# Performance work log

Measured on AMD Instinct MI355X. Metric: run time of the kernel, lower is better.

The kernel has to match this reference:

```python
import jax, jax.numpy as jnp
import numpy as np

B, N, DIM = 2, 2048, 512
HEADS, DIM_HEAD = 8, 64
INNER = HEADS * DIM_HEAD  # 512
SCALE = DIM_HEAD ** -0.5


def setup_inputs() -> dict:
    key = jax.random.key(0)
    k1, k2, k3, k4, k5 = jax.random.split(key, 5)
    s = 0.02
    return {
        "x1": jax.random.normal(k1, (B, N, DIM), jnp.float32),
        "x2": jax.random.normal(k2, (B, N, DIM), jnp.float32),
        "W_qk": jax.random.normal(k3, (DIM, 2 * INNER), jnp.float32) * s,
        "W_v": jax.random.normal(k4, (DIM, INNER), jnp.float32) * s,
        "W_out": jax.random.normal(k5, (INNER, DIM), jnp.float32) * s,
        "b_out": jnp.zeros((DIM,), jnp.float32),
    }


def _split_heads(t):
    # [b, n, h*d] -> [b, h, n, d]
    b, n, _ = t.shape
    return t.reshape(b, n, HEADS, DIM_HEAD).transpose(0, 2, 1, 3)


def reference(x1, x2, W_qk, W_v, W_out, b_out):
    # to_qk(x1) -> chunk into k, v ; to_v(x2) -> q  (names in orig are swapped)
    kv = x1 @ W_qk                      # [b, n1, 2*inner]
    k, v = jnp.split(kv, 2, axis=-1)
    q = x2 @ W_v                        # [b, n2, inner]
    q, k, v = _split_heads(q), _split_heads(k), _split_heads(v)  # [b,h,n,d]
    dots = jnp.einsum("bhid,bhjd->bhij", q, k) * SCALE  # [b,h,n2,n1]
    attn = jax.nn.softmax(dots, axis=-1)
    out = jnp.einsum("bhij,bhjd->bhid", attn, v)         # [b,h,n2,d]
    out = out.transpose(0, 2, 1, 3).reshape(out.shape[0], out.shape[2], INNER)
    return out @ W_out + b_out          # [b, n2, dim]
```

## Files before the change

kernel.cpp:

```cpp
#include <hip/hip_runtime.h>

typedef short bf16x8 __attribute__((ext_vector_type(8)));
typedef short bf16x4 __attribute__((ext_vector_type(4)));
typedef float f32x4 __attribute__((ext_vector_type(4)));
typedef float f32x16 __attribute__((ext_vector_type(16)));
typedef unsigned short u16;
typedef unsigned int u32;
typedef u16 u16x8 __attribute__((ext_vector_type(8)));
typedef u16 u16x4 __attribute__((ext_vector_type(4)));

#define DEV __device__ __forceinline__

DEV u16 f2bf(float f) {
  unsigned u = __float_as_uint(f);
  u += 0x7fff + ((u >> 16) & 1);
  return (u16)(u >> 16);
}

DEV int pkbf(float lo, float hi) {
  return __builtin_amdgcn_perm(__float_as_uint(hi) + 0x8000u,
                               __float_as_uint(lo) + 0x8000u, 0x07060302u);
}

#define MFMA16(a, b, c) __builtin_amdgcn_mfma_f32_16x16x32_bf16(a, b, c, 0, 0, 0)
#define MFMA3216(a, b, c) __builtin_amdgcn_mfma_f32_32x32x16_bf16(a, b, c, 0, 0, 0)

#if __has_builtin(__builtin_amdgcn_mfma_f32_32x32x8bf16_1k)
#define HAVE_PV8 1
#define PVMFMA(a, b, c) __builtin_amdgcn_mfma_f32_32x32x8bf16_1k(a, b, c, 0, 0, 0)
#else
#define HAVE_PV8 0
#endif

#if __has_builtin(__builtin_amdgcn_exp2f)
#define QSCALE 0.18033688011112042f
#define EXPFN(x) __builtin_amdgcn_exp2f(x)
#else
#define QSCALE 0.125f
#define EXPFN(x) __expf(x)
#endif

#define GLD16(gp, lp)                                                     \
  __builtin_amdgcn_global_load_lds(                                       \
      (const __attribute__((address_space(1))) u32*)(gp),                 \
      (__attribute__((address_space(3))) u32*)(lp), 16, 0, 0)

#define WAIT_VM0 __builtin_amdgcn_s_waitcnt(0x0F70)
#define WAIT_LGKM0 __builtin_amdgcn_s_waitcnt(0xC07F)

__global__ __launch_bounds__(256) void wprep(
    const float* __restrict__ Wqk, const float* __restrict__ Wv,
    const float* __restrict__ Wout,
    u16* __restrict__ WqkT, u16* __restrict__ WvT, u16* __restrict__ WoutT) {
  __shared__ float tf[32][33];
  int bx = blockIdx.x, t = threadIdx.x;
  const float* src; u16* dst; int Ncols; int id;
  if (bx < 512)      { id = bx;       src = Wqk;  dst = WqkT;  Ncols = 1024; }
  else if (bx < 768) { id = bx - 512; src = Wv;   dst = WvT;   Ncols = 512; }
  else               { id = bx - 768; src = Wout; dst = WoutT; Ncols = 512; }
  int tilesPerRow = Ncols >> 5;
  int tr = id / tilesPerRow, tc = id % tilesPerRow;
  int r0 = tr * 32, c0 = tc * 32;
  {
    int r = t >> 3, c4 = (t & 7) * 4;
    float4 v = *(const float4*)(src + (long)(r0 + r) * Ncols + c0 + c4);
    tf[r][c4] = v.x; tf[r][c4 + 1] = v.y; tf[r][c4 + 2] = v.z; tf[r][c4 + 3] = v.w;
  }
  __syncthreads();
  {
    int c = t >> 3, r4 = (t & 7) * 4;
    u16x4 o;
    o[0] = f2bf(tf[r4][c]); o[1] = f2bf(tf[r4 + 1][c]);
    o[2] = f2bf(tf[r4 + 2][c]); o[3] = f2bf(tf[r4 + 3][c]);
    *(u16x4*)(dst + (long)(c0 + c) * 512 + r0 + r4) = o;
  }
}

__global__ __launch_bounds__(256) void qkv_gemm(
    const float* __restrict__ x1, const float* __restrict__ x2,
    const u16* __restrict__ WqkT, const u16* __restrict__ WvT,
    u16* __restrict__ out_q, u16* __restrict__ out_k, u16* __restrict__ out_vt) {
  __shared__ u16 sA[2][128 * 40];
  __shared__ u16 sB[2][64 * 40];
  int bx = blockIdx.x, t = threadIdx.x;
  bool isQ = bx < 256;
  int bx2 = isQ ? bx : bx - 256;
  const float* Ap = isQ ? x2 : x1;
  const u16* BT = isQ ? WvT : WqkT;
  int m0 = (bx2 & 31) * 128, n0 = (bx2 >> 5) * 64;
  int w = t >> 6, l = t & 63, lm = l & 15, lq = l >> 4;

  f32x4 zero = {0.f, 0.f, 0.f, 0.f};
  f32x4 acc[2][4];
#pragma unroll
  for (int i = 0; i < 2; ++i)
#pragma unroll
    for (int j = 0; j < 4; ++j) acc[i][j] = zero;

  int sm = t >> 2;
  int skc = (t & 3) * 8;
  const float* gAf = Ap + (long)(m0 + sm) * 512 + skc;
  const u16* gB = BT + (long)(n0 + sm) * 512 + skc;

  auto loadA = [&](int kt, int rows) {
    long off = (long)rows * 512 + kt * 32;
    float4 f0 = *(const float4*)(gAf + off);
    float4 f1 = *(const float4*)(gAf + off + 4);
    bf16x8 o;
    o[0] = (short)f2bf(f0.x); o[1] = (short)f2bf(f0.y);
    o[2] = (short)f2bf(f0.z); o[3] = (short)f2bf(f0.w);
    o[4] = (short)f2bf(f1.x); o[5] = (short)f2bf(f1.y);
    o[6] = (short)f2bf(f1.z); o[7] = (short)f2bf(f1.w);
    return o;
  };

  bf16x8 a0 = loadA(0, 0);
  bf16x8 a1 = loadA(0, 64);
  bf16x8 b0 = *(const bf16x8*)(gB);
  *(bf16x8*)(sA[0] + sm * 40 + skc) = a0;
  *(bf16x8*)(sA[0] + (sm + 64) * 40 + skc) = a1;
  *(bf16x8*)(sB[0] + sm * 40 + skc) = b0;
  __syncthreads();

  for (int kt = 0; kt < 16; ++kt) {
    int cur = kt & 1;
    if (kt < 15) {
      a0 = loadA(kt + 1, 0);
      a1 = loadA(kt + 1, 64);
      b0 = *(const bf16x8*)(gB + (kt + 1) * 32);
    }
    bf16x8 af[2], bfr[4];
    af[0] = *(const bf16x8*)(sA[cur] + (w * 32 + lm) * 40 + lq * 8);
    af[1] = *(const bf16x8*)(sA[cur] + (w * 32 + 16 + lm) * 40 + lq * 8);
#pragma unroll
    for (int s = 0; s < 4; ++s)
      bfr[s] = *(const bf16x8*)(sB[cur] + (s * 16 + lm) * 40 + lq * 8);
#pragma unroll
    for (int ms = 0; ms < 2; ++ms)
#pragma unroll
      for (int s = 0; s < 4; ++s)
        acc[ms][s] = MFMA16(af[ms], bfr[s], acc[ms][s]);
    if (kt < 15) {
      int nxt = 1 - cur;
      *(bf16x8*)(sA[nxt] + sm * 40 + skc) = a0;
      *(bf16x8*)(sA[nxt] + (sm + 64) * 40 + skc) = a1;
      *(bf16x8*)(sB[nxt] + sm * 40 + skc) = b0;
    }
    __syncthreads();
  }

#pragma unroll
  for (int ms = 0; ms < 2; ++ms) {
    int gmBase = m0 + w * 32 + ms * 16 + lq * 4;
#pragma unroll
    for (int s = 0; s < 4; ++s) {
      int gc = n0 + s * 16 + lm;
      int b = gmBase >> 11, n = gmBase & 2047;
      if (isQ) {
#pragma unroll
        for (int r = 0; r < 4; ++r)
          out_q[(((long)(b << 3) + (gc >> 6)) * 2048 + n + r) * 64 + (gc & 63)] =
              f2bf(acc[ms][s][r] * QSCALE);
      } else if (gc < 512) {
#pragma unroll
        for (int r = 0; r < 4; ++r)
          out_k[(((long)(b << 3) + (gc >> 6)) * 2048 + n + r) * 64 + (gc & 63)] =
              f2bf(acc[ms][s][r]);
      } else {
        int c = gc - 512, h = c >> 6, d = c & 63;
        u16x4 vv;
#pragma unroll
        for (int r = 0; r < 4; ++r) vv[r] = f2bf(acc[ms][s][r]);
        *(u16x4*)(out_vt + (((long)(b << 3) + h) * 64 + d) * 2048 + n) = vv;
      }
    }
  }
}

__global__ __launch_bounds__(256, 4) void attn(
    const u16* __restrict__ Q, const u16* __restrict__ K,
    const u16* __restrict__ Vt, u16* __restrict__ O) {
  int id = blockIdx.x;
  int bh = id & 15, qt = id >> 4;
  int b = bh >> 3, h = bh & 7;
  const u16* Kh = K + (long)bh * 2048 * 64;
  const u16* Vh = Vt + (long)bh * 64 * 2048;
  int t = threadIdx.x, w = t >> 6, lane = t & 63, ln = lane & 31, hi = lane >> 5;

  __shared__ u16 smem[4][2][2048];
  u16* ktile = smem[w][0];
  u16* vtile = smem[w][1];

  bf16x8 qf[4];
  {
    const u16* qp = Q + (long)bh * 2048 * 64 + (long)(qt * 32 + ln) * 64 + hi * 8;
#pragma unroll
    for (int dc = 0; dc < 4; ++dc) qf[dc] = *(const bf16x8*)(qp + dc * 16);
  }

  f32x16 accO[2];
#pragma unroll
  for (int dt = 0; dt < 2; ++dt)
#pragma unroll
    for (int i = 0; i < 16; ++i) accO[dt][i] = 0.f;
  float dacc = 0.f;

  int l8 = lane & 7, lr8 = lane >> 3;
  int l4 = lane & 3, lr16 = lane >> 2;
  const u16* gK0 = Kh + (long)(w * 512 + lr8) * 64 + (l8 ^ lr8) * 8;
  const u16* gV0 = Vh + (long)lr16 * 2048 + w * 512 + (l4 ^ (lr16 & 3)) * 8;

  auto stage = [&](int jt) {
    const u16* gk = gK0 + (long)jt * 2048;
    const u16* gv = gV0 + jt * 32;
#pragma unroll
    for (int i = 0; i < 4; ++i) {
      GLD16(gk + i * 512, ktile + i * 512);
      GLD16(gv + (long)i * 32768, vtile + i * 512);
    }
  };

  stage(0);
  WAIT_VM0;

  int s7 = ln & 7, s3 = ln & 3;
  for (int jt = 0; jt < 16; ++jt) {
    f32x16 st1, st2;
#pragma unroll
    for (int i = 0; i < 16; ++i) { st1[i] = 0.f; st2[i] = 0.f; }
    bf16x8 kf0 = *(const bf16x8*)(ktile + ln * 64 + ((0 * 2 + hi) ^ s7) * 8);
    bf16x8 kf1 = *(const bf16x8*)(ktile + ln * 64 + ((1 * 2 + hi) ^ s7) * 8);
    bf16x8 kf2 = *(const bf16x8*)(ktile + ln * 64 + ((2 * 2 + hi) ^ s7) * 8);
    bf16x8 kf3 = *(const bf16x8*)(ktile + ln * 64 + ((3 * 2 + hi) ^ s7) * 8);
    st1 = MFMA3216(kf0, qf[0], st1);
    st2 = MFMA3216(kf1, qf[1], st2);
    st1 = MFMA3216(kf2, qf[2], st1);
    st2 = MFMA3216(kf3, qf[3], st2);

    float p[16];
#pragma unroll
    for (int i = 0; i < 16; ++i) {
      float e = EXPFN(st1[i] + st2[i]);
      p[i] = e;
      dacc += e;
    }

#if HAVE_PV8
#pragma unroll
    for (int c = 0; c < 4; ++c) {
      union { int2 i2; bf16x4 v; } u;
      u.i2.x = pkbf(p[c * 4 + 0], p[c * 4 + 1]);
      u.i2.y = pkbf(p[c * 4 + 2], p[c * 4 + 3]);
#pragma unroll
      for (int dt = 0; dt < 2; ++dt) {
        bf16x4 vf = *(const bf16x4*)(vtile + (dt * 32 + ln) * 32 +
                                     ((c ^ s3) * 8) + hi * 4);
        accO[dt] = PVMFMA(vf, u.v, accO[dt]);
      }
    }
#else
#pragma unroll
    for (int c2 = 0; c2 < 2; ++c2) {
      int o0x = pkbf(p[c2 * 8 + 0], p[c2 * 8 + 1]);
      int o0y = pkbf(p[c2 * 8 + 2], p[c2 * 8 + 3]);
      int o1x = pkbf(p[c2 * 8 + 4], p[c2 * 8 + 5]);
      int o1y = pkbf(p[c2 * 8 + 6], p[c2 * 8 + 7]);
      int s0x = __shfl_xor(o0x, 32), s0y = __shfl_xor(o0y, 32);
      int s1x = __shfl_xor(o1x, 32), s1y = __shfl_xor(o1y, 32);
      union { int4 i4; bf16x8 v; } u;
      if (hi) { u.i4.x = s1x; u.i4.y = s1y; u.i4.z = o1x; u.i4.w = o1y; }
      else    { u.i4.x = o0x; u.i4.y = o0y; u.i4.z = s0x; u.i4.w = s0y; }
#pragma unroll
      for (int dt = 0; dt < 2; ++dt) {
        bf16x8 vf = *(const bf16x8*)(vtile + (dt * 32 + ln) * 32 +
                                     (((c2 * 2 + hi) ^ s3) * 8));
        accO[dt] = MFMA3216(vf, u.v, accO[dt]);
      }
    }
#endif

    if (jt < 15) {
      WAIT_LGKM0;
      stage(jt + 1);
      WAIT_VM0;
    }
  }

  __syncthreads();
  float* cb = (float*)&smem[0][0][0];
  if (w != 0) {
    float* sc = cb + (w - 1) * 2112;
#pragma unroll
    for (int dt = 0; dt < 2; ++dt)
#pragma unroll
      for (int i = 0; i < 16; ++i)
        sc[(dt * 16 + i) * 64 + hi * 32 + ln] = accO[dt][i];
    sc[2048 + hi * 32 + ln] = dacc;
  }
  __syncthreads();
  if (w == 0) {
#pragma unroll
    for (int j = 0; j < 3; ++j) {
      float* sc = cb + j * 2112;
#pragma unroll
      for (int dt = 0; dt < 2; ++dt)
#pragma unroll
        for (int i = 0; i < 16; ++i)
          accO[dt][i] += sc[(dt * 16 + i) * 64 + hi * 32 + ln];
      dacc += sc[2048 + hi * 32 + ln];
    }
    dacc += __shfl_xor(dacc, 32);
    float inv = 1.f / dacc;

    u16* Ob = O + ((long)b * 2048 + qt * 32 + ln) * 512 + h * 64;
#pragma unroll
    for (int dt = 0; dt < 2; ++dt)
#pragma unroll
      for (int gq = 0; gq < 4; ++gq) {
        u16x4 o;
#pragma unroll
        for (int rr = 0; rr < 4; ++rr) o[rr] = f2bf(accO[dt][gq * 4 + rr] * inv);
        *(u16x4*)(Ob + dt * 32 + gq * 8 + hi * 4) = o;
      }
  }
}

__global__ __launch_bounds__(128) void out_gemm(
    const u16* __restrict__ A, const u16* __restrict__ BT,
    float* __restrict__ out_f, const float* __restrict__ bias) {
  __shared__ u16 sA[2][64 * 40];
  __shared__ u16 sB[2][32 * 40];
  int t = threadIdx.x, bx = blockIdx.x;
  int m0 = (bx & 63) * 64, n0 = (bx >> 6) * 32;
  int w = t >> 6, l = t & 63, lm = l & 15, lq = l >> 4;

  f32x4 zero = {0.f, 0.f, 0.f, 0.f};
  f32x4 acc[2][2];
#pragma unroll
  for (int i = 0; i < 2; ++i)
#pragma unroll
    for (int j = 0; j < 2; ++j) acc[i][j] = zero;

  int ar = t >> 1, akc = (t & 1) * 16;
  int br = t >> 2, bkc = (t & 3) * 8;
  const u16* gA = A + (long)(m0 + ar) * 512 + akc;
  const u16* gB = BT + (long)(n0 + br) * 512 + bkc;

  bf16x8 a0 = *(const bf16x8*)(gA);
  bf16x8 a1 = *(const bf16x8*)(gA + 8);
  bf16x8 b0 = *(const bf16x8*)(gB);
  *(bf16x8*)(sA[0] + ar * 40 + akc) = a0;
  *(bf16x8*)(sA[0] + ar * 40 + akc + 8) = a1;
  *(bf16x8*)(sB[0] + br * 40 + bkc) = b0;
  __syncthreads();

  for (int kt = 0; kt < 16; ++kt) {
    int cur = kt & 1;
    if (kt < 15) {
      a0 = *(const bf16x8*)(gA + (kt + 1) * 32);
      a1 = *(const bf16x8*)(gA + (kt + 1) * 32 + 8);
      b0 = *(const bf16x8*)(gB + (kt + 1) * 32);
    }
    bf16x8 af[2], bfr[2];
    af[0] = *(const bf16x8*)(sA[cur] + (w * 32 + lm) * 40 + lq * 8);
    af[1] = *(const bf16x8*)(sA[cur] + (w * 32 + 16 + lm) * 40 + lq * 8);
    bfr[0] = *(const bf16x8*)(sB[cur] + (lm)*40 + lq * 8);
    bfr[1] = *(const bf16x8*)(sB[cur] + (16 + lm) * 40 + lq * 8);
#pragma unroll
    for (int ms = 0; ms < 2; ++ms)
#pragma unroll
      for (int s = 0; s < 2; ++s)
        acc[ms][s] = MFMA16(af[ms], bfr[s], acc[ms][s]);
    if (kt < 15) {
      int nxt = 1 - cur;
      *(bf16x8*)(sA[nxt] + ar * 40 + akc) = a0;
      *(bf16x8*)(sA[nxt] + ar * 40 + akc + 8) = a1;
      *(bf16x8*)(sB[nxt] + br * 40 + bkc) = b0;
    }
    __syncthreads();
  }

#pragma unroll
  for (int ms = 0; ms < 2; ++ms) {
    int gmBase = m0 + w * 32 + ms * 16 + lq * 4;
#pragma unroll
    for (int s = 0; s < 2; ++s) {
      int gc = n0 + s * 16 + lm;
      float bv = bias[gc];
#pragma unroll
      for (int r = 0; r < 4; ++r)
        out_f[(long)(gmBase + r) * 512 + gc] = acc[ms][s][r] + bv;
    }
  }
}

extern "C" void kernel_launch(void* const* d_in, const int* in_sizes, int n_in,
                              void* d_out, int out_size, void* d_ws, size_t ws_size,
                              hipStream_t stream) {
  const float* x1 = (const float*)d_in[0];
  const float* x2 = (const float*)d_in[1];
  const float* Wqk = (const float*)d_in[2];
  const float* Wv = (const float*)d_in[3];
  const float* Wout = (const float*)d_in[4];
  const float* bout = (const float*)d_in[5];
  float* out = (float*)d_out;

  u16* ws = (u16*)d_ws;
  const long SZ = 2097152;
  u16* Qw = ws;
  u16* Kw = ws + SZ;
  u16* Vtw = ws + 2 * SZ;
  u16* Ow = ws + 3 * SZ;
  u16* WqkT = ws + 4 * SZ;
  u16* WvT = WqkT + 524288;
  u16* WoutT = WvT + 262144;

  wprep<<<1024, 256, 0, stream>>>(Wqk, Wv, Wout, WqkT, WvT, WoutT);
  qkv_gemm<<<768, 256, 0, stream>>>(x1, x2, WqkT, WvT, Qw, Kw, Vtw);
  attn<<<1024, 256, 0, stream>>>(Qw, Kw, Vtw, Ow);
  out_gemm<<<1024, 128, 0, stream>>>(Ow, WoutT, out, bout);
}
```

Baseline: 130.0 us.

## Pre-convert activations to bf16 and stage GEMM tiles via direct global-to-LDS loads

```diff
diff --git a/kernel.cpp b/kernel.cpp
--- a/kernel.cpp
+++ b/kernel.cpp
@@ -50,10 +50,25 @@
 
 __global__ __launch_bounds__(256) void wprep(
     const float* __restrict__ Wqk, const float* __restrict__ Wv,
-    const float* __restrict__ Wout,
-    u16* __restrict__ WqkT, u16* __restrict__ WvT, u16* __restrict__ WoutT) {
+    const float* __restrict__ Wout, const float* __restrict__ x1,
+    const float* __restrict__ x2,
+    u16* __restrict__ WqkT, u16* __restrict__ WvT, u16* __restrict__ WoutT,
+    u16* __restrict__ x1b, u16* __restrict__ x2b) {
+  int bx = blockIdx.x, t = threadIdx.x;
+  if (bx >= 1024) {
+    int bx2 = bx - 1024;
+    const float* src = (bx2 < 1024) ? x1 : x2;
+    u16* dst = (bx2 < 1024) ? x1b : x2b;
+    long base = (long)(bx2 & 1023) * 2048 + t * 8;
+    float4 a = *(const float4*)(src + base);
+    float4 b = *(const float4*)(src + base + 4);
+    u16x8 o;
+    o[0] = f2bf(a.x); o[1] = f2bf(a.y); o[2] = f2bf(a.z); o[3] = f2bf(a.w);
+    o[4] = f2bf(b.x); o[5] = f2bf(b.y); o[6] = f2bf(b.z); o[7] = f2bf(b.w);
+    *(u16x8*)(dst + base) = o;
+    return;
+  }
   __shared__ float tf[32][33];
-  int bx = blockIdx.x, t = threadIdx.x;
   const float* src; u16* dst; int Ncols; int id;
   if (bx < 512)      { id = bx;       src = Wqk;  dst = WqkT;  Ncols = 1024; }
   else if (bx < 768) { id = bx - 512; src = Wv;   dst = WvT;   Ncols = 512; }
@@ -77,18 +92,18 @@
 }
 
 __global__ __launch_bounds__(256) void qkv_gemm(
-    const float* __restrict__ x1, const float* __restrict__ x2,
+    const u16* __restrict__ x1b, const u16* __restrict__ x2b,
     const u16* __restrict__ WqkT, const u16* __restrict__ WvT,
     u16* __restrict__ out_q, u16* __restrict__ out_k, u16* __restrict__ out_vt) {
-  __shared__ u16 sA[2][128 * 40];
-  __shared__ u16 sB[2][64 * 40];
+  __shared__ u16 sA[2][4096];
+  __shared__ u16 sB[2][2048];
   int bx = blockIdx.x, t = threadIdx.x;
   bool isQ = bx < 256;
   int bx2 = isQ ? bx : bx - 256;
-  const float* Ap = isQ ? x2 : x1;
+  const u16* A = isQ ? x2b : x1b;
   const u16* BT = isQ ? WvT : WqkT;
   int m0 = (bx2 & 31) * 128, n0 = (bx2 >> 5) * 64;
-  int w = t >> 6, l = t & 63, lm = l & 15, lq = l >> 4;
+  int w = t >> 6, lane = t & 63, lm = lane & 15, lq = lane >> 4;
 
   f32x4 zero = {0.f, 0.f, 0.f, 0.f};
   f32x4 acc[2][4];
@@ -97,55 +112,36 @@
 #pragma unroll
     for (int j = 0; j < 4; ++j) acc[i][j] = zero;
 
-  int sm = t >> 2;
-  int skc = (t & 3) * 8;
-  const float* gAf = Ap + (long)(m0 + sm) * 512 + skc;
-  const u16* gB = BT + (long)(n0 + sm) * 512 + skc;
-
-  auto loadA = [&](int kt, int rows) {
-    long off = (long)rows * 512 + kt * 32;
-    float4 f0 = *(const float4*)(gAf + off);
-    float4 f1 = *(const float4*)(gAf + off + 4);
-    bf16x8 o;
-    o[0] = (short)f2bf(f0.x); o[1] = (short)f2bf(f0.y);
-    o[2] = (short)f2bf(f0.z); o[3] = (short)f2bf(f0.w);
-    o[4] = (short)f2bf(f1.x); o[5] = (short)f2bf(f1.y);
-    o[6] = (short)f2bf(f1.z); o[7] = (short)f2bf(f1.w);
-    return o;
+  int gA0 = w * 128 + lane, gA1 = gA0 + 64;
+  const u16* srcA0 = A + (long)(m0 + (gA0 & 127)) * 512 + (gA0 >> 7) * 8;
+  const u16* srcA1 = A + (long)(m0 + (gA1 & 127)) * 512 + (gA1 >> 7) * 8;
+  int gB = w * 64 + lane;
+  const u16* srcB = BT + (long)(n0 + (gB & 63)) * 512 + (gB >> 6) * 8;
+  int ldsA0 = w * 128 * 8, ldsA1 = ldsA0 + 64 * 8, ldsB = w * 64 * 8;
+
+  auto stage = [&](int kt, int buf) {
+    GLD16(srcA0 + kt * 32, &sA[buf][ldsA0]);
+    GLD16(srcA1 + kt * 32, &sA[buf][ldsA1]);
+    GLD16(srcB + kt * 32, &sB[buf][ldsB]);
   };
 
-  bf16x8 a0 = loadA(0, 0);
-  bf16x8 a1 = loadA(0, 64);
-  bf16x8 b0 = *(const bf16x8*)(gB);
-  *(bf16x8*)(sA[0] + sm * 40 + skc) = a0;
-  *(bf16x8*)(sA[0] + (sm + 64) * 40 + skc) = a1;
-  *(bf16x8*)(sB[0] + sm * 40 + skc) = b0;
+  stage(0, 0);
   __syncthreads();
 
   for (int kt = 0; kt < 16; ++kt) {
     int cur = kt & 1;
-    if (kt < 15) {
-      a0 = loadA(kt + 1, 0);
-      a1 = loadA(kt + 1, 64);
-      b0 = *(const bf16x8*)(gB + (kt + 1) * 32);
-    }
+    if (kt < 15) stage(kt + 1, cur ^ 1);
     bf16x8 af[2], bfr[4];
-    af[0] = *(const bf16x8*)(sA[cur] + (w * 32 + lm) * 40 + lq * 8);
-    af[1] = *(const bf16x8*)(sA[cur] + (w * 32 + 16 + lm) * 40 + lq * 8);
+    af[0] = *(const bf16x8*)(&sA[cur][(lq * 128 + w * 32 + lm) * 8]);
+    af[1] = *(const bf16x8*)(&sA[cur][(lq * 128 + w * 32 + 16 + lm) * 8]);
 #pragma unroll
     for (int s = 0; s < 4; ++s)
-      bfr[s] = *(const bf16x8*)(sB[cur] + (s * 16 + lm) * 40 + lq * 8);
+      bfr[s] = *(const bf16x8*)(&sB[cur][(lq * 64 + s * 16 + lm) * 8]);
 #pragma unroll
     for (int ms = 0; ms < 2; ++ms)
 #pragma unroll
       for (int s = 0; s < 4; ++s)
         acc[ms][s] = MFMA16(af[ms], bfr[s], acc[ms][s]);
-    if (kt < 15) {
-      int nxt = 1 - cur;
-      *(bf16x8*)(sA[nxt] + sm * 40 + skc) = a0;
-      *(bf16x8*)(sA[nxt] + (sm + 64) * 40 + skc) = a1;
-      *(bf16x8*)(sB[nxt] + sm * 40 + skc) = b0;
-    }
     __syncthreads();
   }
 
@@ -328,11 +324,11 @@
 __global__ __launch_bounds__(128) void out_gemm(
     const u16* __restrict__ A, const u16* __restrict__ BT,
     float* __restrict__ out_f, const float* __restrict__ bias) {
-  __shared__ u16 sA[2][64 * 40];
-  __shared__ u16 sB[2][32 * 40];
+  __shared__ u16 sA[2][2048];
+  __shared__ u16 sB[2][1024];
   int t = threadIdx.x, bx = blockIdx.x;
   int m0 = (bx & 63) * 64, n0 = (bx >> 6) * 32;
-  int w = t >> 6, l = t & 63, lm = l & 15, lq = l >> 4;
+  int w = t >> 6, lane = t & 63, lm = lane & 15, lq = lane >> 4;
 
   f32x4 zero = {0.f, 0.f, 0.f, 0.f};
   f32x4 acc[2][2];
@@ -341,42 +337,35 @@
 #pragma unroll
     for (int j = 0; j < 2; ++j) acc[i][j] = zero;
 
-  int ar = t >> 1, akc = (t & 1) * 16;
-  int br = t >> 2, bkc = (t & 3) * 8;
-  const u16* gA = A + (long)(m0 + ar) * 512 + akc;
-  const u16* gB = BT + (long)(n0 + br) * 512 + bkc;
-
-  bf16x8 a0 = *(const bf16x8*)(gA);
-  bf16x8 a1 = *(const bf16x8*)(gA + 8);
-  bf16x8 b0 = *(const bf16x8*)(gB);
-  *(bf16x8*)(sA[0] + ar * 40 + akc) = a0;
-  *(bf16x8*)(sA[0] + ar * 40 + akc + 8) = a1;
-  *(bf16x8*)(sB[0] + br * 40 + bkc) = b0;
+  int gA0 = w * 128 + lane, gA1 = gA0 + 64;
+  const u16* srcA0 = A + (long)(m0 + (gA0 & 63)) * 512 + (gA0 >> 6) * 8;
+  const u16* srcA1 = A + (long)(m0 + (gA1 & 63)) * 512 + (gA1 >> 6) * 8;
+  int gB = w * 64 + lane;
+  const u16* srcB = BT + (long)(n0 + (gB & 31)) * 512 + (gB >> 5) * 8;
+  int ldsA0 = w * 128 * 8, ldsA1 = ldsA0 + 64 * 8, ldsB = w * 64 * 8;
+
+  auto stage = [&](int kt, int buf) {
+    GLD16(srcA0 + kt * 32, &sA[buf][ldsA0]);
+    GLD16(srcA1 + kt * 32, &sA[buf][ldsA1]);
+    GLD16(srcB + kt * 32, &sB[buf][ldsB]);
+  };
+
+  stage(0, 0);
   __syncthreads();
 
   for (int kt = 0; kt < 16; ++kt) {
     int cur = kt & 1;
-    if (kt < 15) {
-      a0 = *(const bf16x8*)(gA + (kt + 1) * 32);
-      a1 = *(const bf16x8*)(gA + (kt + 1) * 32 + 8);
-      b0 = *(const bf16x8*)(gB + (kt + 1) * 32);
-    }
+    if (kt < 15) stage(kt + 1, cur ^ 1);
     bf16x8 af[2], bfr[2];
-    af[0] = *(const bf16x8*)(sA[cur] + (w * 32 + lm) * 40 + lq * 8);
-    af[1] = *(const bf16x8*)(sA[cur] + (w * 32 + 16 + lm) * 40 + lq * 8);
-    bfr[0] = *(const bf16x8*)(sB[cur] + (lm)*40 + lq * 8);
-    bfr[1] = *(const bf16x8*)(sB[cur] + (16 + lm) * 40 + lq * 8);
+    af[0] = *(const bf16x8*)(&sA[cur][(lq * 64 + w * 32 + lm) * 8]);
+    af[1] = *(const bf16x8*)(&sA[cur][(lq * 64 + w * 32 + 16 + lm) * 8]);
+    bfr[0] = *(const bf16x8*)(&sB[cur][(lq * 32 + lm) * 8]);
+    bfr[1] = *(const bf16x8*)(&sB[cur][(lq * 32 + 16 + lm) * 8]);
 #pragma unroll
     for (int ms = 0; ms < 2; ++ms)
 #pragma unroll
       for (int s = 0; s < 2; ++s)
         acc[ms][s] = MFMA16(af[ms], bfr[s], acc[ms][s]);
-    if (kt < 15) {
-      int nxt = 1 - cur;
-      *(bf16x8*)(sA[nxt] + ar * 40 + akc) = a0;
-      *(bf16x8*)(sA[nxt] + ar * 40 + akc + 8) = a1;
-      *(bf16x8*)(sB[nxt] + br * 40 + bkc) = b0;
-    }
     __syncthreads();
   }
 
@@ -411,12 +400,14 @@
   u16* Kw = ws + SZ;
   u16* Vtw = ws + 2 * SZ;
   u16* Ow = ws + 3 * SZ;
-  u16* WqkT = ws + 4 * SZ;
+  u16* x1b = ws + 4 * SZ;
+  u16* x2b = ws + 5 * SZ;
+  u16* WqkT = ws + 6 * SZ;
   u16* WvT = WqkT + 524288;
   u16* WoutT = WvT + 262144;
 
-  wprep<<<1024, 256, 0, stream>>>(Wqk, Wv, Wout, WqkT, WvT, WoutT);
-  qkv_gemm<<<768, 256, 0, stream>>>(x1, x2, WqkT, WvT, Qw, Kw, Vtw);
+  wprep<<<3072, 256, 0, stream>>>(Wqk, Wv, Wout, x1, x2, WqkT, WvT, WoutT, x1b, x2b);
+  qkv_gemm<<<768, 256, 0, stream>>>(x1b, x2b, WqkT, WvT, Qw, Kw, Vtw);
   attn<<<1024, 256, 0, stream>>>(Qw, Kw, Vtw, Ow);
   out_gemm<<<1024, 128, 0, stream>>>(Ow, WoutT, out, bout);
 }
```

New measurement: 145.4 us. +11.8%, slower.
